# Performance work log

Measured on AMD Instinct MI355X. Metric: run time of the kernel, lower is better.

The kernel has to match this reference:

```python
import jax, jax.numpy as jnp
import numpy as np


def setup_inputs() -> dict:
    key = jax.random.key(0)
    kX, kW, kb, ks = jax.random.split(key, 4)
    B, C, H = 32, 3, 64
    D = C * H * H  # 12288, lin_proj is Linear(D, D)
    N = 196        # superpixels
    X = jax.random.normal(kX, (B, C, H, H), dtype=jnp.float32)
    # scale weight like torch default init (~1/sqrt(D)) to keep activations sane
    W = jax.random.normal(kW, (D, D), dtype=jnp.float32) * (1.0 / np.sqrt(D))
    b = jax.random.normal(kb, (D,), dtype=jnp.float32) * 0.01
    seg_map = jax.random.randint(ks, (B, H, H), 0, N, dtype=jnp.int32)
    return {"X": X, "W": W, "b": b, "seg_map": seg_map, "superpixels": N}


def reference(X, W, b, seg_map, superpixels):
    B, C, H, Wd = X.shape
    D = C * H * Wd
    # lin_proj over the fully flattened image (as in the torch module)
    x = X.reshape(B, D) @ W.T + b                      # [B, D]
    x = x.reshape(B, C, H * Wd)                        # back to per-pixel channels
    pix = x.transpose(0, 2, 1).reshape(B * H * Wd, C)  # [B*HW, C]
    # offset segment ids so every image gets its own id range
    ids = (seg_map.reshape(B, H * Wd) + jnp.arange(B, dtype=seg_map.dtype)[:, None] * superpixels).reshape(-1)
    nseg = B * superpixels
    sums = jax.ops.segment_sum(pix, ids, num_segments=nseg)                     # [B*N, C]
    cnts = jax.ops.segment_sum(jnp.ones((ids.shape[0],), x.dtype), ids, num_segments=nseg)
    means = sums / jnp.maximum(cnts, 1.0)[:, None]     # masked mean per superpixel per channel
    return means.reshape(B, superpixels, C)            # [B, N_superpixels, in_chans]
```

## Files before the change

### kernel.cpp

```cpp
#include <hip/hip_runtime.h>


#include <hip/hip_bf16.h>

typedef __attribute__((ext_vector_type(8))) short short8;
typedef __attribute__((ext_vector_type(4))) float f32x4;

namespace {
constexpr int BATCH = 32;
constexpr int CH    = 3;
constexpr int HWPIX = 4096;
constexpr int DDIM  = 12288;
constexpr int KDIM  = 12288;
constexpr int NSEG  = 196;

constexpr int ROWS = 64;
constexpr int BK   = 64;
}

__device__ __forceinline__ ushort bf16rne(float f) {
    union { float f; unsigned u; } v; v.f = f;
    const unsigned r = v.u + 0x7fffu + ((v.u >> 16) & 1u);
    return (ushort)(r >> 16);
}

__device__ __forceinline__ void gload16(const void* g, void* l) {
    __builtin_amdgcn_global_load_lds(
        (const __attribute__((address_space(1))) void*)g,
        (__attribute__((address_space(3))) void*)l, 16, 0, 0);
}

__global__ __launch_bounds__(256) void convert_x_kernel(
    const float* __restrict__ X, ushort* __restrict__ Xb)
{
    const int i = (blockIdx.x * 256 + threadIdx.x) * 4;
    const float4 v = *reinterpret_cast<const float4*>(X + i);
    ushort4 o;
    o.x = bf16rne(v.x); o.y = bf16rne(v.y); o.z = bf16rne(v.z); o.w = bf16rne(v.w);
    *reinterpret_cast<ushort4*>(Xb + i) = o;
}

template<int KSPLIT>
__global__ __launch_bounds__(256, 4) void gemm_kernel(
    const float* __restrict__ Wg, const ushort* __restrict__ Xb,
    float* __restrict__ xpart)
{
    constexpr int KRANGE = KDIM / KSPLIT;
    constexpr int NTILE  = KRANGE / BK;

    __shared__ float  wl[2][ROWS * BK];
    __shared__ ushort xl[2][BATCH * BK];

    const int t    = threadIdx.x;
    const int lane = t & 63;
    const int w    = t >> 6;
    const int d0   = blockIdx.x * ROWS;
    const int kb   = blockIdx.y * KRANGE;

    const int rsub = lane >> 4;
    const int cch  = lane & 15;
    const int xrow = w * 8 + (lane >> 3);
    const int xch  = lane & 7;

    f32x4 acc[2];
#pragma unroll
    for (int nt = 0; nt < 2; ++nt) acc[nt] = (f32x4)(0.f);

#define STAGE(buf, tile)                                                     \
    {                                                                        \
        const int k0 = kb + (tile) * BK;                                     \
        _Pragma("unroll")                                                    \
        for (int i = 0; i < 4; ++i) {                                        \
            const int r  = w * 16 + i * 4 + rsub;                            \
            const int cs = cch ^ (r & 7);                                    \
            gload16(Wg + (size_t)(d0 + r) * KDIM + k0 + cs * 4,              \
                    &wl[buf][(w * 16 + i * 4) * BK]);                        \
        }                                                                    \
        {                                                                    \
            const int cs = xch ^ (xrow & 7);                                 \
            gload16(Xb + (size_t)xrow * KDIM + k0 + cs * 8,                  \
                    &xl[buf][(w * 8) * BK]);                                 \
        }                                                                    \
    }

#define COMPUTE(buf)                                                         \
    {                                                                        \
        _Pragma("unroll")                                                    \
        for (int kk = 0; kk < 2; ++kk) {                                     \
            const int R  = w * 16 + (lane & 15);                             \
            const int c0 = kk * 8 + (lane >> 4) * 2;    \
            const float4 f0 = *reinterpret_cast<const float4*>(              \
                &wl[buf][R * BK + ((c0    ) ^ (lane & 7)) * 4]);             \
            const float4 f1 = *reinterpret_cast<const float4*>(              \
                &wl[buf][R * BK + ((c0 + 1) ^ (lane & 7)) * 4]);             \
            short8 a;                                                        \
            a[0] = (short)bf16rne(f0.x); a[1] = (short)bf16rne(f0.y);        \
            a[2] = (short)bf16rne(f0.z); a[3] = (short)bf16rne(f0.w);        \
            a[4] = (short)bf16rne(f1.x); a[5] = (short)bf16rne(f1.y);        \
            a[6] = (short)bf16rne(f1.z); a[7] = (short)bf16rne(f1.w);        \
            _Pragma("unroll")                                                \
            for (int nt = 0; nt < 2; ++nt) {                                 \
                const int b  = nt * 16 + (lane & 15);                        \
                const int xc = (kk * 4 + (lane >> 4)) ^ (b & 7);             \
                const short8 bb = *reinterpret_cast<const short8*>(          \
                    &xl[buf][b * BK + xc * 8]);                              \
                acc[nt] = __builtin_amdgcn_mfma_f32_16x16x32_bf16(           \
                    a, bb, acc[nt], 0, 0, 0);                                \
            }                                                                \
        }                                                                    \
    }

    STAGE(0, 0)
    __syncthreads();
    for (int tile = 0; tile < NTILE; ++tile) {
        const int cur = tile & 1;
        if (tile + 1 < NTILE) STAGE(cur ^ 1, tile + 1)
        COMPUTE(cur)
        __syncthreads();
    }
#undef STAGE
#undef COMPUTE

    float* xp = xpart + (size_t)blockIdx.y * BATCH * DDIM;
#pragma unroll
    for (int nt = 0; nt < 2; ++nt) {
        const int b = nt * 16 + (lane & 15);
        const int m = d0 + w * 16 + (lane >> 4) * 4;
#pragma unroll
        for (int r = 0; r < 4; ++r)
            xp[(size_t)b * DDIM + m + r] = acc[nt][r];
    }
}

template<int KSPLIT>
__global__ __launch_bounds__(256) void aggregate_kernel(
    const float* __restrict__ xpart, const float* __restrict__ bias,
    const int* __restrict__ seg, float* __restrict__ out)
{
    __shared__ float sums[NSEG];
    __shared__ int   hist[NSEG];
    const int b = blockIdx.x / CH;
    const int c = blockIdx.x % CH;
    for (int i = threadIdx.x; i < NSEG; i += 256) { sums[i] = 0.f; hist[i] = 0; }
    __syncthreads();
    const size_t base = (size_t)b * DDIM + c * HWPIX;
    for (int p = threadIdx.x; p < HWPIX; p += 256) {
        const int s = seg[b * HWPIX + p];
        float v = bias[c * HWPIX + p];
#pragma unroll
        for (int ks = 0; ks < KSPLIT; ++ks)
            v += xpart[(size_t)ks * BATCH * DDIM + base + p];
        atomicAdd(&hist[s], 1);
        atomicAdd(&sums[s], v);
    }
    __syncthreads();
    for (int s = threadIdx.x; s < NSEG; s += 256)
        out[(b * NSEG + s) * CH + c] = sums[s] / fmaxf((float)hist[s], 1.f);
}

extern "C" void kernel_launch(void* const* d_in, const int* in_sizes, int n_in,
                              void* d_out, int out_size, void* d_ws, size_t ws_size,
                              hipStream_t stream) {
    const float* X    = (const float*)d_in[0];
    const float* W    = (const float*)d_in[1];
    const float* bias = (const float*)d_in[2];
    const int*   seg  = (const int*)d_in[3];
    float* out = (float*)d_out;

    ushort* Xb    = (ushort*)d_ws;
    float*  xpart = (float*)(Xb + (size_t)BATCH * KDIM);

    convert_x_kernel<<<BATCH * KDIM / (256 * 4), 256, 0, stream>>>(X, Xb);

    const size_t need8 = (size_t)BATCH * KDIM * 2 + (size_t)8 * BATCH * DDIM * 4;
    if (ws_size >= need8) {
        dim3 grid(DDIM / ROWS, 8);
        gemm_kernel<8><<<grid, 256, 0, stream>>>(W, Xb, xpart);
        aggregate_kernel<8><<<BATCH * CH, 256, 0, stream>>>(xpart, bias, seg, out);
    } else {
        dim3 grid(DDIM / ROWS, 4);
        gemm_kernel<4><<<grid, 256, 0, stream>>>(W, Xb, xpart);
        aggregate_kernel<4><<<BATCH * CH, 256, 0, stream>>>(xpart, bias, seg, out);
    }
}
```

Baseline: 141.3 us.

## Deepen GEMM prefetch to two tiles with explicit vmcnt waits; vectorize aggregate loads

The GEMM loop now keeps two tiles in flight: it issues loads for tiles 0 and 1 up front, waits with s_waitcnt vmcnt(5) so only the current tile's loads must land, and refills the freed buffer after computing. The aim is to hide more global-load latency than the old single-prefetch double buffer, which blocked on a full __syncthreads. Separately, the aggregate kernel reads seg, bias and partial sums as 4-wide vectors to cut load instruction count. The hand-coded vmcnt assumes exactly five outstanding loads per tile per thread, which is brittle if the compiler reorders or splits them.

```diff
diff --git a/kernel.cpp b/kernel.cpp
--- a/kernel.cpp
+++ b/kernel.cpp
@@ -111,12 +111,21 @@
     }
 
     STAGE(0, 0)
-    __syncthreads();
+    STAGE(1, 1)
     for (int tile = 0; tile < NTILE; ++tile) {
         const int cur = tile & 1;
-        if (tile + 1 < NTILE) STAGE(cur ^ 1, tile + 1)
+        if (tile + 1 < NTILE) {
+            asm volatile("s_waitcnt vmcnt(5)" ::: "memory");
+        } else {
+            asm volatile("s_waitcnt vmcnt(0)" ::: "memory");
+        }
+        __builtin_amdgcn_s_barrier();
+        asm volatile("" ::: "memory");
         COMPUTE(cur)
-        __syncthreads();
+        asm volatile("s_waitcnt lgkmcnt(0)" ::: "memory");
+        __builtin_amdgcn_s_barrier();
+        asm volatile("" ::: "memory");
+        if (tile + 2 < NTILE) STAGE(cur, tile + 2)
     }
 #undef STAGE
 #undef COMPUTE
@@ -144,14 +153,21 @@
     for (int i = threadIdx.x; i < NSEG; i += 256) { sums[i] = 0.f; hist[i] = 0; }
     __syncthreads();
     const size_t base = (size_t)b * DDIM + c * HWPIX;
-    for (int p = threadIdx.x; p < HWPIX; p += 256) {
-        const int s = seg[b * HWPIX + p];
-        float v = bias[c * HWPIX + p];
-#pragma unroll
-        for (int ks = 0; ks < KSPLIT; ++ks)
-            v += xpart[(size_t)ks * BATCH * DDIM + base + p];
-        atomicAdd(&hist[s], 1);
-        atomicAdd(&sums[s], v);
+#pragma unroll
+    for (int it = 0; it < HWPIX / 1024; ++it) {
+        const int p0 = it * 1024 + threadIdx.x * 4;
+        const int4 s4 = *reinterpret_cast<const int4*>(seg + b * HWPIX + p0);
+        float4 v = *reinterpret_cast<const float4*>(bias + c * HWPIX + p0);
+#pragma unroll
+        for (int ks = 0; ks < KSPLIT; ++ks) {
+            const float4 xv = *reinterpret_cast<const float4*>(
+                xpart + (size_t)ks * BATCH * DDIM + base + p0);
+            v.x += xv.x; v.y += xv.y; v.z += xv.z; v.w += xv.w;
+        }
+        atomicAdd(&hist[s4.x], 1); atomicAdd(&sums[s4.x], v.x);
+        atomicAdd(&hist[s4.y], 1); atomicAdd(&sums[s4.y], v.y);
+        atomicAdd(&hist[s4.z], 1); atomicAdd(&sums[s4.z], v.z);
+        atomicAdd(&hist[s4.w], 1); atomicAdd(&sums[s4.w], v.w);
     }
     __syncthreads();
     for (int s = threadIdx.x; s < NSEG; s += 256)
```

Result: faster. 135.0 us (-4.5%).
